# Optimization experiments

Hardware: AMD Instinct MI355X
Metric: run time of the kernel (lower is better)

The kernel has to match this reference:

```python
import jax, jax.numpy as jnp
import numpy as np

LOOKUP_WINDOW = 101  # module init arg
EPS = 1e-12  # F.normalize eps


def setup_inputs() -> dict:
    key = jax.random.key(0)
    k1, k2, k3 = jax.random.split(key, 3)
    B, T, F_IN, D = 4, 2048, 2048, 128
    x = jax.random.normal(k1, (B, T, F_IN), dtype=jnp.float32)
    # nn.Linear(in_filters, output_dim); stored here as [in, out] so y = x @ W + b
    W = jax.random.normal(k2, (F_IN, D), dtype=jnp.float32) / np.sqrt(F_IN).astype(np.float32)
    b = jax.random.normal(k3, (D,), dtype=jnp.float32) * 0.01
    return {"x": x, "W": W, "b": b}


def reference(x, W, b):
    hw = LOOKUP_WINDOW // 2
    # projection + L2 normalize over feature dim (F.normalize p=2, dim=-1)
    p = x @ W + b  # [B,T,D]
    p = p / jnp.maximum(jnp.linalg.norm(p, axis=-1, keepdims=True), EPS)
    B, T, D = p.shape
    # zero-pad along time so out-of-range neighbors contribute 0 similarity
    pp = jnp.pad(p, ((0, 0), (hw, hw), (0, 0)))  # [B, T+2*hw, D]
    # window gather: idx[t, w] = t + w indexes padded time axis (neighbor t + w - hw)
    idx = jnp.arange(T)[:, None] + jnp.arange(LOOKUP_WINDOW)[None, :]  # [T, W]
    windows = pp[:, idx, :]  # [B, T, W, D]
    # banded similarity: sim[b,t,w] = <p[b,t], neighbor at offset w-hw>
    sim = jnp.einsum('btd,btwd->btw', p, windows)
    return sim  # [B, T, LOOKUP_WINDOW]
```

## Files before the change

kernel.cpp:

```cpp
#include <hip/hip_runtime.h>
#include <hip/hip_bf16.h>

#define T_LEN 2048
#define D_DIM 128
#define K_DIM 2048
#define M_DIM 8192
#define LOOKUP 101
#define HWIN 50

typedef __attribute__((ext_vector_type(8))) short short8;
typedef __attribute__((ext_vector_type(4))) float f32x4;

static __device__ __forceinline__ unsigned int f2bf(float f) {
  unsigned int u = __float_as_uint(f);
  return (u + 0x7fffu + ((u >> 16) & 1u)) >> 16;
}

static __device__ __forceinline__ short8 pack8(float4 lo, float4 hi) {
  uint4 u;
  u.x = f2bf(lo.x) | (f2bf(lo.y) << 16);
  u.y = f2bf(lo.z) | (f2bf(lo.w) << 16);
  u.z = f2bf(hi.x) | (f2bf(hi.y) << 16);
  u.w = f2bf(hi.z) | (f2bf(hi.w) << 16);
  return *(short8*)&u;
}

typedef __attribute__((address_space(3))) unsigned char lds_uchar;
typedef const __attribute__((address_space(1))) unsigned char g_uchar;
static __device__ __forceinline__ void gll16(const void* g, void* l) {
  __builtin_amdgcn_global_load_lds((g_uchar*)g, (lds_uchar*)l, 16, 0, 0);
}

__global__ __launch_bounds__(256) void k_pack(const float* __restrict__ W,
                                              unsigned short* __restrict__ Bp) {
  __shared__ float sw[32][132];
  const int ks = blockIdx.x;
  const int t = threadIdx.x;
  const float* src = W + (size_t)ks * 32 * D_DIM;
#pragma unroll
  for (int j = 0; j < 4; ++j) {
    int idx = t + j * 256;
    int row = idx >> 5, c4 = idx & 31;
    float4 v = *(const float4*)(src + row * D_DIM + c4 * 4);
    *(float4*)&sw[row][c4 * 4] = v;
  }
  __syncthreads();
#pragma unroll
  for (int e = 0; e < 2; ++e) {
    int f = t * 2 + e;
    int ct = f >> 6, l = f & 63;
    int kr = (l >> 4) * 8, col = ct * 16 + (l & 15);
    uint4 o;
    o.x = f2bf(sw[kr + 0][col]) | (f2bf(sw[kr + 1][col]) << 16);
    o.y = f2bf(sw[kr + 2][col]) | (f2bf(sw[kr + 3][col]) << 16);
    o.z = f2bf(sw[kr + 4][col]) | (f2bf(sw[kr + 5][col]) << 16);
    o.w = f2bf(sw[kr + 6][col]) | (f2bf(sw[kr + 7][col]) << 16);
    *(uint4*)(Bp + (((size_t)(ks * 8 + ct) << 6) + l) * 8) = o;
  }
}

#define CHK 64
#define NCHK (K_DIM / CHK)
#define SLOT 24576

__global__ __launch_bounds__(512, 2) void k_gemm(const float* __restrict__ X,
                                                 const unsigned short* __restrict__ Bp,
                                                 const float* __restrict__ bias,
                                                 unsigned short* __restrict__ Pn) {
  __shared__ __align__(16) unsigned char ring[4 * SLOT + 16384];
  const int tid = threadIdx.x;
  const int lane = tid & 63;
  const int wv = tid >> 6;
  const int r0 = blockIdx.x * 32;
  const int l15 = lane & 15;
  const int kg = lane >> 4;
  const int rg = wv >> 2;
  const int wc = wv & 3;

  f32x4 acc[2];
  acc[0] = (f32x4){0.f, 0.f, 0.f, 0.f};
  acc[1] = (f32x4){0.f, 0.f, 0.f, 0.f};

  auto stage = [&](int cc) {
    unsigned char* base = ring + (cc & 3) * SLOT;
#pragma unroll
    for (int u = 0; u < 3; ++u) {
      int i = wv * 3 + u;
      if (i < 8) {
        int row = i * 4 + (lane >> 4);
        int gs = (lane & 15) ^ (row & 15);
        gll16(X + (size_t)(r0 + row) * K_DIM + cc * CHK + gs * 4, base + i * 1024);
      } else {
        int j = i - 8;
        int ksg = cc * 2 + (j >> 3);
        gll16(Bp + (((size_t)(ksg * 8 + (j & 7))) * 64 + lane) * 8, base + 8192 + j * 1024);
      }
    }
  };

  stage(0);
  stage(1);
  for (int c = 0; c < NCHK; ++c) {
    if (c + 2 < NCHK) {
      stage(c + 2);
      asm volatile("s_waitcnt vmcnt(6)" ::: "memory");
    } else if (c + 1 < NCHK) {
      asm volatile("s_waitcnt vmcnt(3)" ::: "memory");
    } else {
      asm volatile("s_waitcnt vmcnt(0)" ::: "memory");
    }
    __builtin_amdgcn_s_barrier();
    const unsigned char* Ab = ring + (c & 3) * SLOT;
    const unsigned char* Bb = Ab + 8192;
#pragma unroll
    for (int s = 0; s < 2; ++s) {
      int row = rg * 16 + l15;
      int g = kg * 2 + s * 8;
      float4 alo = *(const float4*)(Ab + row * 256 + ((g ^ (row & 15)) << 4));
      float4 ahi = *(const float4*)(Ab + row * 256 + (((g + 1) ^ (row & 15)) << 4));
      short8 af = pack8(alo, ahi);
      short8 w0 = *(const short8*)(Bb + ((s * 8 + wc * 2 + 0) * 64 + lane) * 16);
      short8 w1 = *(const short8*)(Bb + ((s * 8 + wc * 2 + 1) * 64 + lane) * 16);
      acc[0] = __builtin_amdgcn_mfma_f32_16x16x32_bf16(w0, af, acc[0], 0, 0, 0);
      acc[1] = __builtin_amdgcn_mfma_f32_16x16x32_bf16(w1, af, acc[1], 0, 0, 0);
    }
  }

  unsigned char* Pq = ring + 4 * SLOT;
  {
    int row = rg * 16 + l15;
#pragma unroll
    for (int ctl = 0; ctl < 2; ++ctl) {
      int gq = (wc * 2 + ctl) * 4 + kg;
      int byte = row * 512 + ((gq * 16) ^ ((row & 7) << 4));
      *(float4*)(Pq + byte) = make_float4(acc[ctl][0], acc[ctl][1], acc[ctl][2], acc[ctl][3]);
    }
  }
  __syncthreads();

  const int row = tid >> 4;
  const int c8 = tid & 15;
  float4 v0 = *(const float4*)(Pq + row * 512 + (((2 * c8) * 16) ^ ((row & 7) << 4)));
  float4 v1 = *(const float4*)(Pq + row * 512 + (((2 * c8 + 1) * 16) ^ ((row & 7) << 4)));
  float4 bv0 = *(const float4*)(bias + c8 * 8);
  float4 bv1 = *(const float4*)(bias + c8 * 8 + 4);
  float tot[8] = {v0.x + bv0.x, v0.y + bv0.y, v0.z + bv0.z, v0.w + bv0.w,
                  v1.x + bv1.x, v1.y + bv1.y, v1.z + bv1.z, v1.w + bv1.w};
  float ss = 0.f;
#pragma unroll
  for (int i = 0; i < 8; ++i) ss += tot[i] * tot[i];
  ss += __shfl_xor(ss, 1);
  ss += __shfl_xor(ss, 2);
  ss += __shfl_xor(ss, 4);
  ss += __shfl_xor(ss, 8);
  float sc = 1.0f / fmaxf(sqrtf(ss), 1e-12f);
  uint4 o;
  o.x = f2bf(tot[0] * sc) | (f2bf(tot[1] * sc) << 16);
  o.y = f2bf(tot[2] * sc) | (f2bf(tot[3] * sc) << 16);
  o.z = f2bf(tot[4] * sc) | (f2bf(tot[5] * sc) << 16);
  o.w = f2bf(tot[6] * sc) | (f2bf(tot[7] * sc) << 16);
  *(uint4*)(Pn + (size_t)(r0 + row) * D_DIM + c8 * 8) = o;
}

#define SROWS 144

__global__ __launch_bounds__(256) void k_sim(const unsigned short* __restrict__ Pn,
                                             float* __restrict__ out) {
  __shared__ unsigned short sm[SROWS * D_DIM];
  const int bb = blockIdx.x >> 6;
  const int tb = blockIdx.x & 63;
  const int t0 = tb * 32;
  const int tid = threadIdx.x;

  for (int idx = tid; idx < SROWS * 16; idx += 256) {
    int i = idx >> 4, seg = idx & 15;
    int t = t0 - HWIN + i;
    uint4 val = make_uint4(0u, 0u, 0u, 0u);
    if (t >= 0 && t < T_LEN)
      val = *(const uint4*)(Pn + ((size_t)bb * T_LEN + t) * D_DIM + seg * 8);
    *(uint4*)&sm[i * D_DIM + ((seg ^ (i & 7)) << 3)] = val;
  }
  __syncthreads();

  const int lane = tid & 63;
  const int wv = tid >> 6;
  const int l15 = lane & 15;
  const int kg = lane >> 4;
  const int rt = wv >> 1;
  const int itp = wv & 1;

  short8 af[4];
  const int ia = HWIN + rt * 16 + l15;
#pragma unroll
  for (int ks = 0; ks < 4; ++ks) {
    int g = ks * 4 + kg;
    af[ks] = *(const short8*)&sm[ia * D_DIM + ((g ^ (ia & 7)) << 3)];
  }

  for (int it = itp; it < 9; it += 2) {
    f32x4 acc = (f32x4){0.f, 0.f, 0.f, 0.f};
    const int ib = it * 16 + l15;
#pragma unroll
    for (int ks = 0; ks < 4; ++ks) {
      int g = ks * 4 + kg;
      short8 bf = *(const short8*)&sm[ib * D_DIM + ((g ^ (ib & 7)) << 3)];
      acc = __builtin_amdgcn_mfma_f32_16x16x32_bf16(af[ks], bf, acc, 0, 0, 0);
    }
#pragma unroll
    for (int j = 0; j < 4; ++j) {
      int r = rt * 16 + kg * 4 + j;
      int w = ib - r;
      if (w >= 0 && w <= 100)
        out[((size_t)bb * T_LEN + t0 + r) * LOOKUP + w] = acc[j];
    }
  }
}

extern "C" void kernel_launch(void* const* d_in, const int* in_sizes, int n_in,
                              void* d_out, int out_size, void* d_ws, size_t ws_size,
                              hipStream_t stream) {
  (void)in_sizes; (void)n_in; (void)out_size; (void)ws_size;
  const float* x = (const float*)d_in[0];
  const float* W = (const float*)d_in[1];
  const float* b = (const float*)d_in[2];
  float* out = (float*)d_out;
  unsigned short* Bp = (unsigned short*)d_ws;
  unsigned short* Pn = Bp + (size_t)D_DIM * K_DIM;

  k_pack<<<64, 256, 0, stream>>>(W, Bp);
  k_gemm<<<M_DIM / 32, 512, 0, stream>>>(x, Bp, b, Pn);
  k_sim<<<4 * (T_LEN / 32), 256, 0, stream>>>(Pn, out);
}
```

Measured before the change: 40.05 us.

## Load packed W directly into registers and shrink GEMM tile to 16 rows

The projection GEMM now uses 16-row tiles with 256 threads and 512 blocks, and the K chunk grows to 128. The packed bf16 weight fragments are loaded straight from global memory into double-buffered registers instead of being staged through LDS. Only X goes through the async LDS ring, and the MFMA phase is wrapped in s_setprio. This cuts LDS traffic and footprint and raises block count for occupancy, but every block now re-reads the full weight matrix from L2, and register pressure grows from the 16 buffered short8 fragments.

```diff
diff --git a/kernel.cpp b/kernel.cpp
--- a/kernel.cpp
+++ b/kernel.cpp
@@ -59,89 +59,90 @@
   }
 }
 
-#define CHK 64
+#define CHK 128
 #define NCHK (K_DIM / CHK)
-#define SLOT 24576
-
-__global__ __launch_bounds__(512, 2) void k_gemm(const float* __restrict__ X,
+
+__global__ __launch_bounds__(256, 2) void k_gemm(const float* __restrict__ X,
                                                  const unsigned short* __restrict__ Bp,
                                                  const float* __restrict__ bias,
                                                  unsigned short* __restrict__ Pn) {
-  __shared__ __align__(16) unsigned char ring[4 * SLOT + 16384];
+  __shared__ __align__(16) unsigned char ring[4 * 8192 + 8192];
   const int tid = threadIdx.x;
   const int lane = tid & 63;
   const int wv = tid >> 6;
-  const int r0 = blockIdx.x * 32;
+  const int r0 = blockIdx.x * 16;
   const int l15 = lane & 15;
   const int kg = lane >> 4;
-  const int rg = wv >> 2;
-  const int wc = wv & 3;
+  const int wc = wv;
 
   f32x4 acc[2];
   acc[0] = (f32x4){0.f, 0.f, 0.f, 0.f};
   acc[1] = (f32x4){0.f, 0.f, 0.f, 0.f};
 
   auto stage = [&](int cc) {
-    unsigned char* base = ring + (cc & 3) * SLOT;
-#pragma unroll
-    for (int u = 0; u < 3; ++u) {
-      int i = wv * 3 + u;
-      if (i < 8) {
-        int row = i * 4 + (lane >> 4);
-        int gs = (lane & 15) ^ (row & 15);
-        gll16(X + (size_t)(r0 + row) * K_DIM + cc * CHK + gs * 4, base + i * 1024);
-      } else {
-        int j = i - 8;
-        int ksg = cc * 2 + (j >> 3);
-        gll16(Bp + (((size_t)(ksg * 8 + (j & 7))) * 64 + lane) * 8, base + 8192 + j * 1024);
-      }
+    unsigned char* base = ring + (cc & 3) * 8192;
+#pragma unroll
+    for (int u = 0; u < 2; ++u) {
+      int idx = wv * 2 + u;
+      int row = idx * 2 + (lane >> 5);
+      int gs = (lane & 31) ^ (row & 7);
+      gll16(X + (size_t)(r0 + row) * K_DIM + cc * CHK + gs * 4, base + idx * 1024);
     }
   };
+#define LOADB(P, cc)                                                                     \
+  {                                                                                      \
+    _Pragma("unroll") for (int q = 0; q < 4; ++q) {                                      \
+      _Pragma("unroll") for (int t = 0; t < 2; ++t)                                      \
+          P[q * 2 + t] = *(const short8*)(Bp +                                           \
+              (((size_t)((cc) * 4 + q) * 8 + (wc * 2 + t)) * 64 + lane) * 8);            \
+    }                                                                                    \
+  }
+
+  short8 breg[2][8];
 
   stage(0);
+  LOADB(breg[0], 0);
   stage(1);
+
+#pragma unroll
   for (int c = 0; c < NCHK; ++c) {
-    if (c + 2 < NCHK) {
-      stage(c + 2);
-      asm volatile("s_waitcnt vmcnt(6)" ::: "memory");
-    } else if (c + 1 < NCHK) {
-      asm volatile("s_waitcnt vmcnt(3)" ::: "memory");
+    if (c + 1 < NCHK) LOADB(breg[(c + 1) & 1], c + 1);
+    if (c + 2 < NCHK) stage(c + 2);
+    if (c <= NCHK - 3) {
+      asm volatile("s_waitcnt vmcnt(12)" ::: "memory");
+    } else if (c == NCHK - 2) {
+      asm volatile("s_waitcnt vmcnt(10)" ::: "memory");
     } else {
       asm volatile("s_waitcnt vmcnt(0)" ::: "memory");
     }
     __builtin_amdgcn_s_barrier();
-    const unsigned char* Ab = ring + (c & 3) * SLOT;
-    const unsigned char* Bb = Ab + 8192;
-#pragma unroll
-    for (int s = 0; s < 2; ++s) {
-      int row = rg * 16 + l15;
-      int g = kg * 2 + s * 8;
-      float4 alo = *(const float4*)(Ab + row * 256 + ((g ^ (row & 15)) << 4));
-      float4 ahi = *(const float4*)(Ab + row * 256 + (((g + 1) ^ (row & 15)) << 4));
+    const unsigned char* Ab = ring + (c & 3) * 8192;
+    __builtin_amdgcn_s_setprio(1);
+#pragma unroll
+    for (int s = 0; s < 4; ++s) {
+      int g0 = s * 8 + kg * 2;
+      float4 alo = *(const float4*)(Ab + l15 * 512 + ((g0 ^ (l15 & 7)) << 4));
+      float4 ahi = *(const float4*)(Ab + l15 * 512 + (((g0 + 1) ^ (l15 & 7)) << 4));
       short8 af = pack8(alo, ahi);
-      short8 w0 = *(const short8*)(Bb + ((s * 8 + wc * 2 + 0) * 64 + lane) * 16);
-      short8 w1 = *(const short8*)(Bb + ((s * 8 + wc * 2 + 1) * 64 + lane) * 16);
-      acc[0] = __builtin_amdgcn_mfma_f32_16x16x32_bf16(w0, af, acc[0], 0, 0, 0);
-      acc[1] = __builtin_amdgcn_mfma_f32_16x16x32_bf16(w1, af, acc[1], 0, 0, 0);
-    }
-  }
-
-  unsigned char* Pq = ring + 4 * SLOT;
-  {
-    int row = rg * 16 + l15;
-#pragma unroll
-    for (int ctl = 0; ctl < 2; ++ctl) {
-      int gq = (wc * 2 + ctl) * 4 + kg;
-      int byte = row * 512 + ((gq * 16) ^ ((row & 7) << 4));
-      *(float4*)(Pq + byte) = make_float4(acc[ctl][0], acc[ctl][1], acc[ctl][2], acc[ctl][3]);
-    }
+      acc[0] = __builtin_amdgcn_mfma_f32_16x16x32_bf16(breg[c & 1][s * 2 + 0], af, acc[0], 0, 0, 0);
+      acc[1] = __builtin_amdgcn_mfma_f32_16x16x32_bf16(breg[c & 1][s * 2 + 1], af, acc[1], 0, 0, 0);
+    }
+    __builtin_amdgcn_s_setprio(0);
+  }
+
+  unsigned char* Pq = ring + 4 * 8192;
+#pragma unroll
+  for (int ctl = 0; ctl < 2; ++ctl) {
+    int gq = (wc * 2 + ctl) * 4 + kg;
+    int byte = l15 * 512 + ((gq << 4) ^ ((l15 & 7) << 4));
+    *(float4*)(Pq + byte) = make_float4(acc[ctl][0], acc[ctl][1], acc[ctl][2], acc[ctl][3]);
   }
   __syncthreads();
 
   const int row = tid >> 4;
   const int c8 = tid & 15;
-  float4 v0 = *(const float4*)(Pq + row * 512 + (((2 * c8) * 16) ^ ((row & 7) << 4)));
-  float4 v1 = *(const float4*)(Pq + row * 512 + (((2 * c8 + 1) * 16) ^ ((row & 7) << 4)));
+  float4 v0 = *(const float4*)(Pq + row * 512 + (((2 * c8) << 4) ^ ((row & 7) << 4)));
+  float4 v1 = *(const float4*)(Pq + row * 512 + (((2 * c8 + 1) << 4) ^ ((row & 7) << 4)));
   float4 bv0 = *(const float4*)(bias + c8 * 8);
   float4 bv1 = *(const float4*)(bias + c8 * 8 + 4);
   float tot[8] = {v0.x + bv0.x, v0.y + bv0.y, v0.z + bv0.z, v0.w + bv0.w,
@@ -228,6 +229,6 @@
   unsigned short* Pn = Bp + (size_t)D_DIM * K_DIM;
 
   k_pack<<<64, 256, 0, stream>>>(W, Bp);
-  k_gemm<<<M_DIM / 32, 512, 0, stream>>>(x, Bp, b, Pn);
+  k_gemm<<<M_DIM / 16, 256, 0, stream>>>(x, Bp, b, Pn);
   k_sim<<<4 * (T_LEN / 32), 256, 0, stream>>>(Pn, out);
 }
```

After: 34.61 us. -13.6%, faster.
